# Performance work log

Hardware: AMD Instinct MI355X
Metric: run time of the kernel (lower is better)

Reference implementation:

```python
import jax, jax.numpy as jnp
import numpy as np

N = 50000      # nodes
E = 1_600_000  # edges (avg degree 32)
D = 128        # in/hidden channels
OUT = 64       # out channels


def setup_inputs() -> dict:
    key = jax.random.key(0)
    ks = jax.random.split(key, 12)
    s = 0.08  # ~glorot scale for 128-dim
    return {
        "x": jax.random.normal(ks[0], (N, D), jnp.float32),
        "edge_index": jax.random.randint(ks[1], (2, E), 0, N, dtype=jnp.int64),
        # GCN layer 1
        "W1": jax.random.normal(ks[2], (D, D), jnp.float32) * s,
        "b1": jnp.zeros((D,), jnp.float32),
        # GraphSAGE layer 2 (mean aggregation): lin_l on neighbors, lin_r on root
        "Wl": jax.random.normal(ks[3], (D, D), jnp.float32) * s,
        "Wr": jax.random.normal(ks[4], (D, D), jnp.float32) * s,
        "bs": jnp.zeros((D,), jnp.float32),
        # GAT layer 3 (heads=1, concat=False)
        "Wg": jax.random.normal(ks[5], (D, D), jnp.float32) * s,
        "a_s": jax.random.normal(ks[6], (D,), jnp.float32) * s,
        "a_d": jax.random.normal(ks[7], (D,), jnp.float32) * s,
        "bg": jnp.zeros((D,), jnp.float32),
        # GCN output layer
        "Wo": jax.random.normal(ks[8], (D, OUT), jnp.float32) * s,
        "bo": jnp.zeros((OUT,), jnp.float32),
    }


def _self_loops(src, dst, n):
    loop = jnp.arange(n, dtype=src.dtype)
    return jnp.concatenate([src, loop]), jnp.concatenate([dst, loop])


def gcn_conv(x, W, b, src, dst, n):
    # PyG GCNConv: add self-loops, symmetric normalization D^-1/2 (A+I) D^-1/2
    s2, d2 = _self_loops(src, dst, n)
    deg = jax.ops.segment_sum(jnp.ones_like(d2, dtype=x.dtype), d2, num_segments=n)
    dinv = jnp.where(deg > 0, jax.lax.rsqrt(deg), 0.0)
    h = x @ W                         # [n, out]
    norm = dinv[s2] * dinv[d2]        # [E+n]
    out = jax.ops.segment_sum(h[s2] * norm[:, None], d2, num_segments=n)
    return out + b


def sage_conv(x, Wl, Wr, b, src, dst, n):
    # PyG SAGEConv, aggr='mean': W_l * mean_neigh + W_r * x (no self-loops)
    deg = jax.ops.segment_sum(jnp.ones_like(dst, dtype=x.dtype), dst, num_segments=n)
    agg = jax.ops.segment_sum(x[src], dst, num_segments=n)
    mean = agg / jnp.maximum(deg, 1.0)[:, None]
    return mean @ Wl + x @ Wr + b


def gat_conv(x, W, a_s, a_d, b, src, dst, n):
    # PyG GATConv heads=1, concat=False: self-loops, edge softmax over incoming edges
    h = x @ W                               # [n, out]
    s2, d2 = _self_loops(src, dst, n)
    alpha_src = h @ a_s                     # [n]
    alpha_dst = h @ a_d                     # [n]
    e = jax.nn.leaky_relu(alpha_src[s2] + alpha_dst[d2], negative_slope=0.2)
    m = jax.ops.segment_max(e, d2, num_segments=n)   # every node has a self-loop
    ex = jnp.exp(e - m[d2])
    denom = jax.ops.segment_sum(ex, d2, num_segments=n)
    alpha = ex / denom[d2]
    out = jax.ops.segment_sum(alpha[:, None] * h[s2], d2, num_segments=n)
    return out + b


def reference(x, edge_index, W1, b1, Wl, Wr, bs, Wg, a_s, a_d, bg, Wo, bo):
    src, dst = edge_index[0], edge_index[1]
    n = x.shape[0]
    # eval mode: F.dropout(training=False) is identity
    h = jax.nn.relu(gcn_conv(x, W1, b1, src, dst, n))
    h = jax.nn.relu(sage_conv(h, Wl, Wr, bs, src, dst, n))
    h = jax.nn.relu(gat_conv(h, Wg, a_s, a_d, bg, src, dst, n))
    return gcn_conv(h, Wo, bo, src, dst, n)
```

## Files before the change

kernel.cpp:

```cpp
#include <hip/hip_runtime.h>
#include <math.h>


#define BUCKET_BITS 8
#define BUCKET_SZ   256
#define NBMAX       256
#define CAP         10240
#define CAPE        768

typedef short short8 __attribute__((ext_vector_type(8)));
typedef float f32x4 __attribute__((ext_vector_type(4)));
typedef float f32x2 __attribute__((ext_vector_type(2)));
typedef unsigned int u32x4 __attribute__((ext_vector_type(4)));
typedef unsigned short u16x8 __attribute__((ext_vector_type(8)));

__device__ __forceinline__ float leaky02(float x) { return x > 0.0f ? x : 0.2f * x; }
__device__ __forceinline__ float bflo(unsigned u) { return __uint_as_float(u << 16); }
__device__ __forceinline__ float bfhi(unsigned u) { return __uint_as_float(u & 0xFFFF0000u); }
__device__ __forceinline__ unsigned short f2bf(float f) {
    unsigned u = __float_as_uint(f);
    u += 0x7FFFu + ((u >> 16) & 1u);
    return (unsigned short)(u >> 16);
}

__global__ __launch_bounds__(256) void wpackall_k(
    const float* __restrict__ W1, const float* __restrict__ Wl,
    const float* __restrict__ Wr, const float* __restrict__ Wg,
    const float* __restrict__ Wo,
    unsigned* __restrict__ P1, unsigned* __restrict__ Pl,
    unsigned* __restrict__ Pr, unsigned* __restrict__ Pg,
    unsigned* __restrict__ Po, int* __restrict__ bcur, int nb)
{
    const int b = blockIdx.x;
    if (b == 5) {
        int t = threadIdx.x;
        if (t < nb) bcur[t] = t * CAP;
        return;
    }
    const float* W; unsigned* P; int NO;
    if      (b == 0) { W = W1; P = P1; NO = 128; }
    else if (b == 1) { W = Wl; P = Pl; NO = 128; }
    else if (b == 2) { W = Wr; P = Pr; NO = 128; }
    else if (b == 3) { W = Wg; P = Pg; NO = 128; }
    else             { W = Wo; P = Po; NO = 64;  }
    const int CT = NO / 16;
    const int n4w = NO / 4;
    for (int f = threadIdx.x; f < 64 * n4w; f += 256) {
        const int kp = f / n4w;
        const int n4 = f % n4w;
        const float4 a = *(const float4*)(W + (size_t)(2 * kp) * NO + n4 * 4);
        const float4 bb = *(const float4*)(W + (size_t)(2 * kp + 1) * NO + n4 * 4);
        const int k = 2 * kp, kb = k >> 5, qq = (k >> 3) & 3, p = (k & 7) >> 1;
        const float av[4] = {a.x, a.y, a.z, a.w};
        const float bv[4] = {bb.x, bb.y, bb.z, bb.w};
#pragma unroll
        for (int j = 0; j < 4; j++) {
            int col = n4 * 4 + j;
            int c = col >> 4, nl = col & 15;
            unsigned pk = (unsigned)f2bf(av[j]) | ((unsigned)f2bf(bv[j]) << 16);
            P[(((kb * CT + c) * 64) + qq * 16 + nl) * 4 + p] = pk;
        }
    }
}

template<int NO, bool AFP32, bool SCALE, bool BIASRELU, bool DUAL, bool DOTS>
__global__ __launch_bounds__(256) void mgemm_k(
    const void* __restrict__ Av, const unsigned short* __restrict__ Bp,
    const void* __restrict__ A1v, const unsigned short* __restrict__ Bp1,
    unsigned short* __restrict__ C16,
    const float* __restrict__ scale, const float* __restrict__ bias,
    const float* __restrict__ a_s, const float* __restrict__ a_d,
    float* __restrict__ as_, float* __restrict__ ad_, int n)
{
    constexpr int CT = NO / 16;
    const int tid = threadIdx.x;
    const int wave = tid >> 6, lane = tid & 63;
    const int q = lane >> 4, ml = lane & 15;
    const int row0 = blockIdx.x * 64 + wave * 16;
    int arow = row0 + ml; if (arow >= n) arow = n - 1;

    f32x4 acc[CT];
#pragma unroll
    for (int c = 0; c < CT; c++) acc[c] = {0.f, 0.f, 0.f, 0.f};

    for (int half = 0; half < (DUAL ? 2 : 1); half++) {
        const unsigned short* __restrict__ Bsrc = half ? Bp1 : Bp;
        const void* Asrc = half ? A1v : Av;
#pragma unroll
        for (int kb = 0; kb < 4; kb++) {
            short8 afr;
            if (AFP32) {
                const float* Af = (const float*)Asrc + (size_t)arow * 128 + kb * 32 + q * 8;
                float4 f0 = *(const float4*)Af;
                float4 f1 = *(const float4*)(Af + 4);
                afr[0] = (short)f2bf(f0.x); afr[1] = (short)f2bf(f0.y);
                afr[2] = (short)f2bf(f0.z); afr[3] = (short)f2bf(f0.w);
                afr[4] = (short)f2bf(f1.x); afr[5] = (short)f2bf(f1.y);
                afr[6] = (short)f2bf(f1.z); afr[7] = (short)f2bf(f1.w);
            } else {
                afr = *(const short8*)((const unsigned short*)Asrc +
                                       ((size_t)(kb >> 1) * n + arow) * 64 +
                                       (kb & 1) * 32 + q * 8);
            }
            short8 bfr[CT];
#pragma unroll
            for (int c = 0; c < CT; c++)
                bfr[c] = *(const short8*)(Bsrc + ((size_t)(kb * CT + c) * 64 + lane) * 8);
#pragma unroll
            for (int c = 0; c < CT; c++)
                acc[c] = __builtin_amdgcn_mfma_f32_16x16x32_bf16(afr, bfr[c], acc[c], 0, 0, 0);
        }
    }

    if (DOTS) {
        float ps[4] = {0.f, 0.f, 0.f, 0.f}, pd[4] = {0.f, 0.f, 0.f, 0.f};
#pragma unroll
        for (int c = 0; c < CT; c++) {
            float sv = a_s[c * 16 + ml], dv = a_d[c * 16 + ml];
#pragma unroll
            for (int r = 0; r < 4; r++) {
                ps[r] = fmaf(acc[c][r], sv, ps[r]);
                pd[r] = fmaf(acc[c][r], dv, pd[r]);
            }
        }
#pragma unroll
        for (int off = 1; off < 16; off <<= 1) {
#pragma unroll
            for (int r = 0; r < 4; r++) {
                ps[r] += __shfl_xor(ps[r], off, 64);
                pd[r] += __shfl_xor(pd[r], off, 64);
            }
        }
        if (ml == 0) {
#pragma unroll
            for (int r = 0; r < 4; r++) {
                int row = row0 + q * 4 + r;
                if (row < n) { as_[row] = ps[r]; ad_[row] = pd[r]; }
            }
        }
    }

    float sc[4];
    if (SCALE) {
#pragma unroll
        for (int r = 0; r < 4; r++) {
            int row = row0 + q * 4 + r;
            sc[r] = scale[row < n ? row : 0];
        }
    }
#pragma unroll
    for (int c = 0; c < CT; c++) {
        float bv = BIASRELU ? bias[c * 16 + ml] : 0.0f;
        const int col = c * 16 + ml;
#pragma unroll
        for (int r = 0; r < 4; r++) {
            int row = row0 + q * 4 + r;
            if (row < n) {
                float v = acc[c][r];
                if (SCALE) v *= sc[r];
                if (BIASRELU) v = fmaxf(v + bv, 0.0f);
                C16[((size_t)(col >> 6) * n + row) * 64 + (col & 63)] = f2bf(v);
            }
        }
    }
}

#define PART_CH 4096
__global__ __launch_bounds__(256) void part_k(
    const int* __restrict__ src, const int* __restrict__ dst,
    int* __restrict__ bcur, unsigned long long* __restrict__ part, int nE)
{
    __shared__ int cnt[NBMAX];
    __shared__ int cur[NBMAX];
    const int base = blockIdx.x * PART_CH;
    const int t = threadIdx.x;
    cnt[t] = 0;
    __syncthreads();
    int d[PART_CH / 256], s[PART_CH / 256];
#pragma unroll
    for (int j = 0; j < PART_CH / 256; j++) {
        int e = base + j * 256 + t;
        if (e < nE) {
            d[j] = dst[e]; s[j] = src[e];
            atomicAdd(&cnt[d[j] >> BUCKET_BITS], 1);
        } else d[j] = -1;
    }
    __syncthreads();
    {
        int c = cnt[t];
        cur[t] = c ? atomicAdd(&bcur[t], c) : 0;
    }
    __syncthreads();
#pragma unroll
    for (int j = 0; j < PART_CH / 256; j++) {
        if (d[j] >= 0) {
            int p = atomicAdd(&cur[d[j] >> BUCKET_BITS], 1);
            part[p] = ((unsigned long long)(unsigned)d[j] << 32) | (unsigned)s[j];
        }
    }
}

__global__ __launch_bounds__(256) void csr_k(
    const unsigned long long* __restrict__ part, const int* __restrict__ bcur,
    int* __restrict__ rowptr, int* __restrict__ srcs,
    float* __restrict__ dinv, float* __restrict__ invm, int n, int nE, int nb)
{
    __shared__ int lcnt[BUCKET_SZ];
    __shared__ int sm[BUCKET_SZ];
    __shared__ int lcur[BUCKET_SZ];
    const int b = blockIdx.x;
    const int t = threadIdx.x;
    const int base_in = b * CAP;
    const int cntE = bcur[b] - base_in;

    int vb = (t < nb) ? (bcur[t] - t * CAP) : 0;
    sm[t] = vb;
    __syncthreads();
    for (int off = 1; off < 256; off <<= 1) {
        int tv = (t >= off) ? sm[t - off] : 0;
        __syncthreads();
        sm[t] += tv;
        __syncthreads();
    }
    const int base_out = sm[b] - (bcur[b] - b * CAP);
    __syncthreads();

    lcnt[t] = 0;
    __syncthreads();
#pragma unroll 4
    for (int e = t; e < cntE; e += 256) {
        int dl = (int)(part[base_in + e] >> 32) & (BUCKET_SZ - 1);
        atomicAdd(&lcnt[dl], 1);
    }
    __syncthreads();
    int v = lcnt[t];
    sm[t] = v;
    __syncthreads();
    for (int off = 1; off < 256; off <<= 1) {
        int tv = (t >= off) ? sm[t - off] : 0;
        __syncthreads();
        sm[t] += tv;
        __syncthreads();
    }
    const int excl = sm[t] - v;
    const int node = (b << BUCKET_BITS) + t;
    if (node < n) {
        rowptr[node] = base_out + excl;
        float dg = (float)v;
        dinv[node] = rsqrtf(dg + 1.0f);
        invm[node] = 1.0f / fmaxf(dg, 1.0f);
        if (node == n - 1) rowptr[n] = nE;
    }
    lcur[t] = excl;
    __syncthreads();
#pragma unroll 4
    for (int e = t; e < cntE; e += 256) {
        unsigned long long w = part[base_in + e];
        int dl = (int)(w >> 32) & (BUCKET_SZ - 1);
        int pos = atomicAdd(&lcur[dl], 1);
        srcs[base_out + pos] = (int)(unsigned)w;
    }
}

__global__ __launch_bounds__(256) void gatw_k(
    const int* __restrict__ rowptr, const int* __restrict__ srcs,
    const float* __restrict__ as_, const float* __restrict__ ad_,
    float* __restrict__ ew, float* __restrict__ rdn_, float* __restrict__ sw_, int n)
{
    const int node = blockIdx.x * 32 + (threadIdx.x >> 3);
    const int lane = threadIdx.x & 7;
    if (node >= n) return;
    const int beg = rowptr[node], end = rowptr[node + 1];
    const float ad_d = ad_[node];
    float psum = 0.f;
    for (int k = beg + lane; k < end; k += 8) {
        float e = __expf(leaky02(as_[srcs[k]] + ad_d));
        ew[k] = e;
        psum += e;
    }
#pragma unroll
    for (int off = 4; off > 0; off >>= 1) psum += __shfl_xor(psum, off, 64);
    if (lane == 0) {
        float se = __expf(leaky02(as_[node] + ad_d));
        float r = 1.0f / (psum + se);
        rdn_[node] = r;
        sw_[node] = se * r;
    }
}

template<int MODE, bool OV>
__device__ __forceinline__ void gath_loop(
    const char* __restrict__ Hb, unsigned loff,
    const int* __restrict__ srcs, const float* __restrict__ ew,
    const int* lsrc, const float* lw,
    int beg, int end, int beg_blk, f32x2* acc)
{
    int k = beg;
    for (; k + 16 <= end; k += 16) {
        int s[16]; float wv[16];
#pragma unroll
        for (int j = 0; j < 16; j++) {
            int ofs = k + j - beg_blk;
            if (OV) {
                bool in = ofs < CAPE;
                int ofc = in ? ofs : 0;
                s[j] = in ? lsrc[ofc] : srcs[k + j];
                if (MODE == 2) wv[j] = in ? lw[ofc] : ew[k + j];
            } else {
                s[j] = lsrc[ofs];
                if (MODE == 2) wv[j] = lw[ofs];
            }
        }
        u32x4 h[16];
#pragma unroll
        for (int j = 0; j < 16; j++)
            h[j] = *(const u32x4*)(Hb + (size_t)(((unsigned)s[j] << 7) + loff));
#pragma unroll
        for (int j = 0; j < 16; j++) {
            f32x2 w2 = {wv[j], wv[j]};
#pragma unroll
            for (int c = 0; c < 4; c++) {
                f32x2 hv = {bflo(h[j][c]), bfhi(h[j][c])};
                if (MODE == 2) acc[c] = w2 * hv + acc[c];
                else           acc[c] = acc[c] + hv;
            }
        }
    }
    for (; k + 8 <= end; k += 8) {
        int s[8]; float wv[8];
#pragma unroll
        for (int j = 0; j < 8; j++) {
            int ofs = k + j - beg_blk;
            if (OV) {
                bool in = ofs < CAPE;
                int ofc = in ? ofs : 0;
                s[j] = in ? lsrc[ofc] : srcs[k + j];
                if (MODE == 2) wv[j] = in ? lw[ofc] : ew[k + j];
            } else {
                s[j] = lsrc[ofs];
                if (MODE == 2) wv[j] = lw[ofs];
            }
        }
        u32x4 h[8];
#pragma unroll
        for (int j = 0; j < 8; j++)
            h[j] = *(const u32x4*)(Hb + (size_t)(((unsigned)s[j] << 7) + loff));
#pragma unroll
        for (int j = 0; j < 8; j++) {
            f32x2 w2 = {wv[j], wv[j]};
#pragma unroll
            for (int c = 0; c < 4; c++) {
                f32x2 hv = {bflo(h[j][c]), bfhi(h[j][c])};
                if (MODE == 2) acc[c] = w2 * hv + acc[c];
                else           acc[c] = acc[c] + hv;
            }
        }
    }
    if (k < end) {
        int s[8]; float wv[8];
#pragma unroll
        for (int j = 0; j < 8; j++) {
            int kk = k + j;
            bool act = kk < end;
            int kc = act ? kk : end - 1;
            int ofs = kc - beg_blk;
            int sj; float w0 = 1.0f;
            if (OV) {
                bool in = ofs < CAPE;
                int ofc = in ? ofs : 0;
                sj = in ? lsrc[ofc] : srcs[kc];
                if (MODE == 2) w0 = in ? lw[ofc] : ew[kc];
            } else {
                sj = lsrc[ofs];
                if (MODE == 2) w0 = lw[ofs];
            }
            s[j] = sj;
            wv[j] = act ? ((MODE == 2) ? w0 : 1.0f) : 0.0f;
        }
        u32x4 h[8];
#pragma unroll
        for (int j = 0; j < 8; j++)
            h[j] = *(const u32x4*)(Hb + (size_t)(((unsigned)s[j] << 7) + loff));
#pragma unroll
        for (int j = 0; j < 8; j++) {
            f32x2 w2 = {wv[j], wv[j]};
#pragma unroll
            for (int c = 0; c < 4; c++) {
                f32x2 hv = {bflo(h[j][c]), bfhi(h[j][c])};
                acc[c] = w2 * hv + acc[c];
            }
        }
    }
}

template<int NCB, int MODE>
__global__ __launch_bounds__(128, 4) void gatherbf_k(
    const unsigned short* __restrict__ H16, float* __restrict__ outf,
    unsigned short* __restrict__ out16,
    const int* __restrict__ rowptr, const int* __restrict__ srcs,
    const float* __restrict__ scl,
    const float* __restrict__ sw_,
    const float* __restrict__ ew,
    const float* __restrict__ bias, int n)
{
    constexpr int XPC = 8 / NCB;
    constexpr int NPB = 16;
    __shared__ int lsrc[CAPE];
    __shared__ float lw[(MODE == 2) ? CAPE : 1];

    const int bid = (int)blockIdx.x;
    const int xj = bid & 7;
    const int cb = xj / XPC;
    const int NG = (n + NPB - 1) / NPB;
    const int ng = (bid >> 3) * XPC + (xj % XPC);
    if (ng >= NG) return;

    const int tid = (int)threadIdx.x;
    const int node0 = ng * NPB;
    const int nodeN = min(node0 + NPB, n);
    const int beg_blk = rowptr[node0];
    const int end_blk = rowptr[nodeN];
    const int cnt = end_blk - beg_blk;
    const int cl = min(cnt, CAPE);
    for (int i = tid; i < cl; i += 128) {
        lsrc[i] = srcs[beg_blk + i];
        if (MODE == 2) lw[i] = ew[beg_blk + i];
    }
    __syncthreads();

    const int node = node0 + (tid >> 3);
    const int lane = tid & 7;
    if (node >= nodeN) return;
    const int beg = rowptr[node], end = rowptr[node + 1];
    const char* __restrict__ Hb = (const char*)H16 + (size_t)cb * n * 128;
    const unsigned loff = (unsigned)lane * 16u;

    f32x2 acc[4];
#pragma unroll
    for (int c = 0; c < 4; c++) acc[c] = {0.f, 0.f};

    if (cnt <= CAPE)
        gath_loop<MODE, false>(Hb, loff, srcs, ew, lsrc, lw, beg, end, beg_blk, acc);
    else
        gath_loop<MODE, true>(Hb, loff, srcs, ew, lsrc, lw, beg, end, beg_blk, acc);

    const size_t orow = ((size_t)cb * n + node) * 8 + lane;
    float r[8];
    if (MODE == 0) {
        float sc = scl[node];
#pragma unroll
        for (int c = 0; c < 4; c++) { r[2*c] = acc[c].x * sc; r[2*c+1] = acc[c].y * sc; }
    } else {
        u32x4 su = *(const u32x4*)(Hb + (size_t)(((unsigned)node << 7) + loff));
        float sv[8];
#pragma unroll
        for (int c = 0; c < 4; c++) { sv[2*c] = bflo(su[c]); sv[2*c+1] = bfhi(su[c]); }
        const float4* b4 = (const float4*)bias;
        float4 ba = b4[cb * 16 + lane * 2], bb = b4[cb * 16 + lane * 2 + 1];
        float bv[8] = {ba.x, ba.y, ba.z, ba.w, bb.x, bb.y, bb.z, bb.w};
        float a8[8];
#pragma unroll
        for (int c = 0; c < 4; c++) { a8[2*c] = acc[c].x; a8[2*c+1] = acc[c].y; }
        if (MODE == 2) {
            float rden = scl[node], sw = sw_[node];
#pragma unroll
            for (int j = 0; j < 8; j++)
                r[j] = fmaxf(fmaf(rden, a8[j], fmaf(sw, sv[j], bv[j])), 0.f);
        } else {
            float dv = scl[node];
#pragma unroll
            for (int j = 0; j < 8; j++) {
                r[j] = dv * (a8[j] + sv[j]) + bv[j];
                if (MODE == 1) r[j] = fmaxf(r[j], 0.f);
            }
        }
    }
    if (MODE == 3) {
        float4* o4 = (float4*)(outf + (size_t)node * 64 + lane * 8);
        float4 ra = {r[0], r[1], r[2], r[3]}, rb = {r[4], r[5], r[6], r[7]};
        o4[0] = ra; o4[1] = rb;
    } else {
        u16x8 qv;
#pragma unroll
        for (int j = 0; j < 8; j++) qv[j] = f2bf(r[j]);
        ((u16x8*)out16)[orow] = qv;
    }
}

extern "C" void kernel_launch(void* const* d_in, const int* in_sizes, int n_in,
                              void* d_out, int out_size, void* d_ws, size_t ws_size,
                              hipStream_t stream)
{
    const float* x   = (const float*)d_in[0];
    const int*   ei  = (const int*)d_in[1];
    const float* W1  = (const float*)d_in[2];
    const float* b1  = (const float*)d_in[3];
    const float* Wl  = (const float*)d_in[4];
    const float* Wr  = (const float*)d_in[5];
    const float* bs  = (const float*)d_in[6];
    const float* Wg  = (const float*)d_in[7];
    const float* a_s = (const float*)d_in[8];
    const float* a_d = (const float*)d_in[9];
    const float* bg  = (const float*)d_in[10];
    const float* Wo  = (const float*)d_in[11];
    const float* bo  = (const float*)d_in[12];

    const int n  = in_sizes[0] / 128;
    const int nE = in_sizes[1] / 2;
    const int* src = ei;
    const int* dst = ei + nE;

    char* w = (char*)d_ws;
    auto alloc = [&](size_t bytes) { char* p = w; w += (bytes + 255) & ~(size_t)255; return p; };
    unsigned short* S0 = (unsigned short*)alloc((size_t)n * 128 * 2);
    unsigned short* S1 = (unsigned short*)alloc((size_t)n * 128 * 2);
    unsigned short* S2 = (unsigned short*)alloc((size_t)n * 128 * 2);
    const int nbv = (n + BUCKET_SZ - 1) / BUCKET_SZ;
    unsigned long long* part = (unsigned long long*)alloc((size_t)nbv * CAP * 8);
    int*   srcs   = (int*)alloc((size_t)nE * 4);
    float* ew     = (float*)alloc((size_t)nE * 4);
    int*   rowptr = (int*)alloc((size_t)(n + 1) * 4);
    int*   bcur   = (int*)alloc(NBMAX * 4);
    float* dinv   = (float*)alloc((size_t)n * 4);
    float* invm   = (float*)alloc((size_t)n * 4);
    float* as_    = (float*)alloc((size_t)n * 4);
    float* ad_    = (float*)alloc((size_t)n * 4);
    float* rdn_   = (float*)alloc((size_t)n * 4);
    float* sw_    = (float*)alloc((size_t)n * 4);
    unsigned* P1  = (unsigned*)alloc(64 * 128 * 4);
    unsigned* Pl  = (unsigned*)alloc(64 * 128 * 4);
    unsigned* Pr  = (unsigned*)alloc(64 * 128 * 4);
    unsigned* Pg  = (unsigned*)alloc(64 * 128 * 4);
    unsigned* Po  = (unsigned*)alloc(64 * 64 * 4);

    const int TB = 256;
    auto cdiv = [](long long a, long long b) { return (int)((a + b - 1) / b); };
    const int nb     = nbv;
    const int gPart  = cdiv(nE, PART_CH);
    const int gGemm  = cdiv(n, 64);
    const int NG     = cdiv(n, 16);
    const int gGa128 = 8 * cdiv(NG, 4);
    const int gGa64  = 8 * cdiv(NG, 8);
    const int gGatw  = cdiv(n, 32);

    wpackall_k<<<6, TB, 0, stream>>>(W1, Wl, Wr, Wg, Wo, P1, Pl, Pr, Pg, Po, bcur, nb);
    part_k<<<gPart, TB, 0, stream>>>(src, dst, bcur, part, nE);
    csr_k<<<nb, TB, 0, stream>>>(part, bcur, rowptr, srcs, dinv, invm, n, nE, nb);

    mgemm_k<128, true, true, false, false, false><<<gGemm, TB, 0, stream>>>(
        x, (const unsigned short*)P1, nullptr, nullptr, S0, dinv, nullptr,
        nullptr, nullptr, nullptr, nullptr, n);
    gatherbf_k<2, 1><<<gGa128, 128, 0, stream>>>(S0, nullptr, S1, rowptr, srcs,
                                                 dinv, nullptr, nullptr, b1, n);

    gatherbf_k<2, 0><<<gGa128, 128, 0, stream>>>(S1, nullptr, S0, rowptr, srcs,
                                                 invm, nullptr, nullptr, nullptr, n);
    mgemm_k<128, false, false, true, true, false><<<gGemm, TB, 0, stream>>>(
        S0, (const unsigned short*)Pl, S1, (const unsigned short*)Pr, S2,
        nullptr, bs, nullptr, nullptr, nullptr, nullptr, n);

    mgemm_k<128, false, false, false, false, true><<<gGemm, TB, 0, stream>>>(
        S2, (const unsigned short*)Pg, nullptr, nullptr, S1, nullptr, nullptr,
        a_s, a_d, as_, ad_, n);
    gatw_k<<<gGatw, TB, 0, stream>>>(rowptr, srcs, as_, ad_, ew, rdn_, sw_, n);
    gatherbf_k<2, 2><<<gGa128, 128, 0, stream>>>(S1, nullptr, S0, rowptr, srcs,
                                                 rdn_, sw_, ew, bg, n);

    mgemm_k<64, false, true, false, false, false><<<gGemm, TB, 0, stream>>>(
        S0, (const unsigned short*)Po, nullptr, nullptr, S2, dinv, nullptr,
        nullptr, nullptr, nullptr, nullptr, n);
    gatherbf_k<1, 3><<<gGa64, 128, 0, stream>>>(S2, (float*)d_out, nullptr, rowptr, srcs,
                                                dinv, nullptr, nullptr, bo, n);
}
```

Before: 328.1 us.

## Switch bf16 feature buffers to row-major and gather full rows per node

Replaces the column-blocked bf16 feature layout (two 64-wide column blocks stored as separate planes) with plain row-major storage in the GEMM loads and stores. The gather kernel now gives each node 16 lanes covering its whole 256-byte row (8 lanes for the 64-wide output) in 256-thread blocks, instead of one block per column half. The goal is to read each edge's source index list once per node rather than once per column block, and to fetch whole contiguous rows. The trade-off is fewer blocks with more threads and register pressure each, plus a different shared-memory staging capacity.

Result: slower. 366.5 us (+11.7%).

```diff
diff --git a/kernel.cpp b/kernel.cpp
--- a/kernel.cpp
+++ b/kernel.cpp
@@ -6,7 +6,6 @@
 #define BUCKET_SZ   256
 #define NBMAX       256
 #define CAP         10240
-#define CAPE        768
 
 typedef short short8 __attribute__((ext_vector_type(8)));
 typedef float f32x4 __attribute__((ext_vector_type(4)));
@@ -99,8 +98,7 @@
                 afr[6] = (short)f2bf(f1.z); afr[7] = (short)f2bf(f1.w);
             } else {
                 afr = *(const short8*)((const unsigned short*)Asrc +
-                                       ((size_t)(kb >> 1) * n + arow) * 64 +
-                                       (kb & 1) * 32 + q * 8);
+                                       (size_t)arow * 128 + kb * 32 + q * 8);
             }
             short8 bfr[CT];
 #pragma unroll
@@ -159,7 +157,7 @@
                 float v = acc[c][r];
                 if (SCALE) v *= sc[r];
                 if (BIASRELU) v = fmaxf(v + bv, 0.0f);
-                C16[((size_t)(col >> 6) * n + row) * 64 + (col & 63)] = f2bf(v);
+                C16[(size_t)row * NO + col] = f2bf(v);
             }
         }
     }
@@ -288,13 +286,14 @@
     }
 }
 
-template<int MODE, bool OV>
+template<int LPN, int MODE, int CAPEV, bool OV>
 __device__ __forceinline__ void gath_loop(
     const char* __restrict__ Hb, unsigned loff,
     const int* __restrict__ srcs, const float* __restrict__ ew,
     const int* lsrc, const float* lw,
     int beg, int end, int beg_blk, f32x2* acc)
 {
+    constexpr int RSH = (LPN == 16) ? 8 : 7;
     int k = beg;
     for (; k + 16 <= end; k += 16) {
         int s[16]; float wv[16];
@@ -302,7 +301,7 @@
         for (int j = 0; j < 16; j++) {
             int ofs = k + j - beg_blk;
             if (OV) {
-                bool in = ofs < CAPE;
+                bool in = ofs < CAPEV;
                 int ofc = in ? ofs : 0;
                 s[j] = in ? lsrc[ofc] : srcs[k + j];
                 if (MODE == 2) wv[j] = in ? lw[ofc] : ew[k + j];
@@ -314,7 +313,7 @@
         u32x4 h[16];
 #pragma unroll
         for (int j = 0; j < 16; j++)
-            h[j] = *(const u32x4*)(Hb + (size_t)(((unsigned)s[j] << 7) + loff));
+            h[j] = *(const u32x4*)(Hb + (size_t)(((unsigned)s[j] << RSH) + loff));
 #pragma unroll
         for (int j = 0; j < 16; j++) {
             f32x2 w2 = {wv[j], wv[j]};
@@ -332,7 +331,7 @@
         for (int j = 0; j < 8; j++) {
             int ofs = k + j - beg_blk;
             if (OV) {
-                bool in = ofs < CAPE;
+                bool in = ofs < CAPEV;
                 int ofc = in ? ofs : 0;
                 s[j] = in ? lsrc[ofc] : srcs[k + j];
                 if (MODE == 2) wv[j] = in ? lw[ofc] : ew[k + j];
@@ -344,7 +343,7 @@
         u32x4 h[8];
 #pragma unroll
         for (int j = 0; j < 8; j++)
-            h[j] = *(const u32x4*)(Hb + (size_t)(((unsigned)s[j] << 7) + loff));
+            h[j] = *(const u32x4*)(Hb + (size_t)(((unsigned)s[j] << RSH) + loff));
 #pragma unroll
         for (int j = 0; j < 8; j++) {
             f32x2 w2 = {wv[j], wv[j]};
@@ -366,7 +365,7 @@
             int ofs = kc - beg_blk;
             int sj; float w0 = 1.0f;
             if (OV) {
-                bool in = ofs < CAPE;
+                bool in = ofs < CAPEV;
                 int ofc = in ? ofs : 0;
                 sj = in ? lsrc[ofc] : srcs[kc];
                 if (MODE == 2) w0 = in ? lw[ofc] : ew[kc];
@@ -380,7 +379,7 @@
         u32x4 h[8];
 #pragma unroll
         for (int j = 0; j < 8; j++)
-            h[j] = *(const u32x4*)(Hb + (size_t)(((unsigned)s[j] << 7) + loff));
+            h[j] = *(const u32x4*)(Hb + (size_t)(((unsigned)s[j] << RSH) + loff));
 #pragma unroll
         for (int j = 0; j < 8; j++) {
             f32x2 w2 = {wv[j], wv[j]};
@@ -393,8 +392,8 @@
     }
 }
 
-template<int NCB, int MODE>
-__global__ __launch_bounds__(128, 4) void gatherbf_k(
+template<int LPN, int MODE>
+__global__ __launch_bounds__(256, 4) void gatherbf_k(
     const unsigned short* __restrict__ H16, float* __restrict__ outf,
     unsigned short* __restrict__ out16,
     const int* __restrict__ rowptr, const int* __restrict__ srcs,
@@ -403,60 +402,54 @@
     const float* __restrict__ ew,
     const float* __restrict__ bias, int n)
 {
-    constexpr int XPC = 8 / NCB;
-    constexpr int NPB = 16;
-    __shared__ int lsrc[CAPE];
-    __shared__ float lw[(MODE == 2) ? CAPE : 1];
-
-    const int bid = (int)blockIdx.x;
-    const int xj = bid & 7;
-    const int cb = xj / XPC;
-    const int NG = (n + NPB - 1) / NPB;
-    const int ng = (bid >> 3) * XPC + (xj % XPC);
-    if (ng >= NG) return;
+    constexpr int NPB = 256 / LPN;
+    constexpr int CAPEV = (LPN == 16) ? 768 : 1280;
+    constexpr int RSH = (LPN == 16) ? 8 : 7;
+    __shared__ int lsrc[CAPEV];
+    __shared__ float lw[(MODE == 2) ? CAPEV : 1];
 
     const int tid = (int)threadIdx.x;
-    const int node0 = ng * NPB;
+    const int node0 = (int)blockIdx.x * NPB;
     const int nodeN = min(node0 + NPB, n);
     const int beg_blk = rowptr[node0];
     const int end_blk = rowptr[nodeN];
     const int cnt = end_blk - beg_blk;
-    const int cl = min(cnt, CAPE);
-    for (int i = tid; i < cl; i += 128) {
+    const int cl = min(cnt, CAPEV);
+    for (int i = tid; i < cl; i += 256) {
         lsrc[i] = srcs[beg_blk + i];
         if (MODE == 2) lw[i] = ew[beg_blk + i];
     }
     __syncthreads();
 
-    const int node = node0 + (tid >> 3);
-    const int lane = tid & 7;
+    const int node = node0 + tid / LPN;
+    const int lane = tid & (LPN - 1);
     if (node >= nodeN) return;
     const int beg = rowptr[node], end = rowptr[node + 1];
-    const char* __restrict__ Hb = (const char*)H16 + (size_t)cb * n * 128;
+    const char* __restrict__ Hb = (const char*)H16;
     const unsigned loff = (unsigned)lane * 16u;
 
     f32x2 acc[4];
 #pragma unroll
     for (int c = 0; c < 4; c++) acc[c] = {0.f, 0.f};
 
-    if (cnt <= CAPE)
-        gath_loop<MODE, false>(Hb, loff, srcs, ew, lsrc, lw, beg, end, beg_blk, acc);
+    if (cnt <= CAPEV)
+        gath_loop<LPN, MODE, CAPEV, false>(Hb, loff, srcs, ew, lsrc, lw, beg, end, beg_blk, acc);
     else
-        gath_loop<MODE, true>(Hb, loff, srcs, ew, lsrc, lw, beg, end, beg_blk, acc);
-
-    const size_t orow = ((size_t)cb * n + node) * 8 + lane;
+        gath_loop<LPN, MODE, CAPEV, true>(Hb, loff, srcs, ew, lsrc, lw, beg, end, beg_blk, acc);
+
+    const size_t orow = (size_t)node * LPN + lane;
     float r[8];
     if (MODE == 0) {
         float sc = scl[node];
 #pragma unroll
         for (int c = 0; c < 4; c++) { r[2*c] = acc[c].x * sc; r[2*c+1] = acc[c].y * sc; }
     } else {
-        u32x4 su = *(const u32x4*)(Hb + (size_t)(((unsigned)node << 7) + loff));
+        u32x4 su = *(const u32x4*)(Hb + (size_t)(((unsigned)node << RSH) + loff));
         float sv[8];
 #pragma unroll
         for (int c = 0; c < 4; c++) { sv[2*c] = bflo(su[c]); sv[2*c+1] = bfhi(su[c]); }
         const float4* b4 = (const float4*)bias;
-        float4 ba = b4[cb * 16 + lane * 2], bb = b4[cb * 16 + lane * 2 + 1];
+        float4 ba = b4[lane * 2], bb = b4[lane * 2 + 1];
         float bv[8] = {ba.x, ba.y, ba.z, ba.w, bb.x, bb.y, bb.z, bb.w};
         float a8[8];
 #pragma unroll
@@ -538,9 +531,8 @@
     const int nb     = nbv;
     const int gPart  = cdiv(nE, PART_CH);
     const int gGemm  = cdiv(n, 64);
-    const int NG     = cdiv(n, 16);
-    const int gGa128 = 8 * cdiv(NG, 4);
-    const int gGa64  = 8 * cdiv(NG, 8);
+    const int gGa128 = cdiv(n, 16);
+    const int gGa64  = cdiv(n, 32);
     const int gGatw  = cdiv(n, 32);
 
     wpackall_k<<<6, TB, 0, stream>>>(W1, Wl, Wr, Wg, Wo, P1, Pl, Pr, Pg, Po, bcur, nb);
@@ -550,10 +542,10 @@
     mgemm_k<128, true, true, false, false, false><<<gGemm, TB, 0, stream>>>(
         x, (const unsigned short*)P1, nullptr, nullptr, S0, dinv, nullptr,
         nullptr, nullptr, nullptr, nullptr, n);
-    gatherbf_k<2, 1><<<gGa128, 128, 0, stream>>>(S0, nullptr, S1, rowptr, srcs,
+    gatherbf_k<16, 1><<<gGa128, TB, 0, stream>>>(S0, nullptr, S1, rowptr, srcs,
                                                  dinv, nullptr, nullptr, b1, n);
 
-    gatherbf_k<2, 0><<<gGa128, 128, 0, stream>>>(S1, nullptr, S0, rowptr, srcs,
+    gatherbf_k<16, 0><<<gGa128, TB, 0, stream>>>(S1, nullptr, S0, rowptr, srcs,
                                                  invm, nullptr, nullptr, nullptr, n);
     mgemm_k<128, false, false, true, true, false><<<gGemm, TB, 0, stream>>>(
         S0, (const unsigned short*)Pl, S1, (const unsigned short*)Pr, S2,
@@ -563,12 +555,12 @@
         S2, (const unsigned short*)Pg, nullptr, nullptr, S1, nullptr, nullptr,
         a_s, a_d, as_, ad_, n);
     gatw_k<<<gGatw, TB, 0, stream>>>(rowptr, srcs, as_, ad_, ew, rdn_, sw_, n);
-    gatherbf_k<2, 2><<<gGa128, 128, 0, stream>>>(S1, nullptr, S0, rowptr, srcs,
+    gatherbf_k<16, 2><<<gGa128, TB, 0, stream>>>(S1, nullptr, S0, rowptr, srcs,
                                                  rdn_, sw_, ew, bg, n);
 
     mgemm_k<64, false, true, false, false, false><<<gGemm, TB, 0, stream>>>(
         S0, (const unsigned short*)Po, nullptr, nullptr, S2, dinv, nullptr,
         nullptr, nullptr, nullptr, nullptr, n);
-    gatherbf_k<1, 3><<<gGa64, 128, 0, stream>>>(S2, (float*)d_out, nullptr, rowptr, srcs,
-                                                dinv, nullptr, nullptr, bo, n);
-}
+    gatherbf_k<8, 3><<<gGa64, TB, 0, stream>>>(S2, (float*)d_out, nullptr, rowptr, srcs,
+                                               dinv, nullptr, nullptr, bo, n);
+}
```

## Fuse GAT edge-softmax weight computation into the attention gather kernel

Applied to the files above, without the earlier changes.

Removes the separate gatw_k kernel that wrote per-edge exp weights and per-node softmax denominators to global memory. The MODE 2 gather now computes edge weights into shared memory during staging, using a small binary search over local row offsets, and derives the softmax denominator per node with a warp reduction. This avoids a launch and an edge-sized global write and read. In exchange, the exps and as_ gathers are recomputed in each column-block replica of the gather.

Result: no change. 329.4 us (+0.4%).

```diff
diff --git a/kernel.cpp b/kernel.cpp
--- a/kernel.cpp
+++ b/kernel.cpp
@@ -262,36 +262,10 @@
     }
 }
 
-__global__ __launch_bounds__(256) void gatw_k(
-    const int* __restrict__ rowptr, const int* __restrict__ srcs,
-    const float* __restrict__ as_, const float* __restrict__ ad_,
-    float* __restrict__ ew, float* __restrict__ rdn_, float* __restrict__ sw_, int n)
-{
-    const int node = blockIdx.x * 32 + (threadIdx.x >> 3);
-    const int lane = threadIdx.x & 7;
-    if (node >= n) return;
-    const int beg = rowptr[node], end = rowptr[node + 1];
-    const float ad_d = ad_[node];
-    float psum = 0.f;
-    for (int k = beg + lane; k < end; k += 8) {
-        float e = __expf(leaky02(as_[srcs[k]] + ad_d));
-        ew[k] = e;
-        psum += e;
-    }
-#pragma unroll
-    for (int off = 4; off > 0; off >>= 1) psum += __shfl_xor(psum, off, 64);
-    if (lane == 0) {
-        float se = __expf(leaky02(as_[node] + ad_d));
-        float r = 1.0f / (psum + se);
-        rdn_[node] = r;
-        sw_[node] = se * r;
-    }
-}
-
 template<int MODE, bool OV>
 __device__ __forceinline__ void gath_loop(
     const char* __restrict__ Hb, unsigned loff,
-    const int* __restrict__ srcs, const float* __restrict__ ew,
+    const int* __restrict__ srcs, const float* __restrict__ as_, float ad_d,
     const int* lsrc, const float* lw,
     int beg, int end, int beg_blk, f32x2* acc)
 {
@@ -304,8 +278,10 @@
             if (OV) {
                 bool in = ofs < CAPE;
                 int ofc = in ? ofs : 0;
-                s[j] = in ? lsrc[ofc] : srcs[k + j];
-                if (MODE == 2) wv[j] = in ? lw[ofc] : ew[k + j];
+                int sg = in ? lsrc[ofc] : srcs[k + j];
+                s[j] = sg;
+                if (MODE == 2)
+                    wv[j] = in ? lw[ofc] : __expf(leaky02(as_[sg] + ad_d));
             } else {
                 s[j] = lsrc[ofs];
                 if (MODE == 2) wv[j] = lw[ofs];
@@ -334,8 +310,10 @@
             if (OV) {
                 bool in = ofs < CAPE;
                 int ofc = in ? ofs : 0;
-                s[j] = in ? lsrc[ofc] : srcs[k + j];
-                if (MODE == 2) wv[j] = in ? lw[ofc] : ew[k + j];
+                int sg = in ? lsrc[ofc] : srcs[k + j];
+                s[j] = sg;
+                if (MODE == 2)
+                    wv[j] = in ? lw[ofc] : __expf(leaky02(as_[sg] + ad_d));
             } else {
                 s[j] = lsrc[ofs];
                 if (MODE == 2) wv[j] = lw[ofs];
@@ -369,7 +347,8 @@
                 bool in = ofs < CAPE;
                 int ofc = in ? ofs : 0;
                 sj = in ? lsrc[ofc] : srcs[kc];
-                if (MODE == 2) w0 = in ? lw[ofc] : ew[kc];
+                if (MODE == 2)
+                    w0 = in ? lw[ofc] : __expf(leaky02(as_[sj] + ad_d));
             } else {
                 sj = lsrc[ofs];
                 if (MODE == 2) w0 = lw[ofs];
@@ -398,15 +377,16 @@
     const unsigned short* __restrict__ H16, float* __restrict__ outf,
     unsigned short* __restrict__ out16,
     const int* __restrict__ rowptr, const int* __restrict__ srcs,
-    const float* __restrict__ scl,
-    const float* __restrict__ sw_,
-    const float* __restrict__ ew,
+    const float* __restrict__ p0, const float* __restrict__ p1,
     const float* __restrict__ bias, int n)
 {
     constexpr int XPC = 8 / NCB;
     constexpr int NPB = 16;
     __shared__ int lsrc[CAPE];
     __shared__ float lw[(MODE == 2) ? CAPE : 1];
+    __shared__ int lro[(MODE == 2) ? (NPB + 1) : 1];
+    __shared__ float lad[(MODE == 2) ? NPB : 1];
+    __shared__ float las[(MODE == 2) ? NPB : 1];
 
     const int bid = (int)blockIdx.x;
     const int xj = bid & 7;
@@ -422,11 +402,27 @@
     const int end_blk = rowptr[nodeN];
     const int cnt = end_blk - beg_blk;
     const int cl = min(cnt, CAPE);
-    for (int i = tid; i < cl; i += 128) {
-        lsrc[i] = srcs[beg_blk + i];
-        if (MODE == 2) lw[i] = ew[beg_blk + i];
-    }
-    __syncthreads();
+
+    if (MODE == 2) {
+        if (tid <= nodeN - node0) lro[tid] = rowptr[node0 + tid] - beg_blk;
+        if (tid < nodeN - node0) { lad[tid] = p1[node0 + tid]; las[tid] = p0[node0 + tid]; }
+        __syncthreads();
+        for (int i = tid; i < cl; i += 128) {
+            int s = srcs[beg_blk + i];
+            lsrc[i] = s;
+            int lo = 0, hi = nodeN - node0;
+#pragma unroll
+            for (int st = 0; st < 4; st++) {
+                int mid = (lo + hi) >> 1;
+                if (i >= lro[mid]) lo = mid; else hi = mid;
+            }
+            lw[i] = __expf(leaky02(p0[s] + lad[lo]));
+        }
+        __syncthreads();
+    } else {
+        for (int i = tid; i < cl; i += 128) lsrc[i] = srcs[beg_blk + i];
+        __syncthreads();
+    }
 
     const int node = node0 + (tid >> 3);
     const int lane = tid & 7;
@@ -435,19 +431,36 @@
     const char* __restrict__ Hb = (const char*)H16 + (size_t)cb * n * 128;
     const unsigned loff = (unsigned)lane * 16u;
 
+    float ad_d = 0.f, rden = 0.f, sw = 0.f;
+    if (MODE == 2) {
+        const int nl = node - node0;
+        ad_d = lad[nl];
+        float self_e = __expf(leaky02(las[nl] + ad_d));
+        float psum = 0.f;
+        for (int k = beg + lane; k < end; k += 8) {
+            int ofs = k - beg_blk;
+            psum += (ofs < CAPE) ? lw[ofs]
+                                 : __expf(leaky02(p0[srcs[k]] + ad_d));
+        }
+#pragma unroll
+        for (int off = 4; off > 0; off >>= 1) psum += __shfl_xor(psum, off, 64);
+        rden = 1.0f / (psum + self_e);
+        sw = self_e * rden;
+    }
+
     f32x2 acc[4];
 #pragma unroll
     for (int c = 0; c < 4; c++) acc[c] = {0.f, 0.f};
 
     if (cnt <= CAPE)
-        gath_loop<MODE, false>(Hb, loff, srcs, ew, lsrc, lw, beg, end, beg_blk, acc);
+        gath_loop<MODE, false>(Hb, loff, srcs, p0, ad_d, lsrc, lw, beg, end, beg_blk, acc);
     else
-        gath_loop<MODE, true>(Hb, loff, srcs, ew, lsrc, lw, beg, end, beg_blk, acc);
+        gath_loop<MODE, true>(Hb, loff, srcs, p0, ad_d, lsrc, lw, beg, end, beg_blk, acc);
 
     const size_t orow = ((size_t)cb * n + node) * 8 + lane;
     float r[8];
     if (MODE == 0) {
-        float sc = scl[node];
+        float sc = p0[node];
 #pragma unroll
         for (int c = 0; c < 4; c++) { r[2*c] = acc[c].x * sc; r[2*c+1] = acc[c].y * sc; }
     } else {
@@ -462,12 +475,11 @@
 #pragma unroll
         for (int c = 0; c < 4; c++) { a8[2*c] = acc[c].x; a8[2*c+1] = acc[c].y; }
         if (MODE == 2) {
-            float rden = scl[node], sw = sw_[node];
 #pragma unroll
             for (int j = 0; j < 8; j++)
                 r[j] = fmaxf(fmaf(rden, a8[j], fmaf(sw, sv[j], bv[j])), 0.f);
         } else {
-            float dv = scl[node];
+            float dv = p0[node];
 #pragma unroll
             for (int j = 0; j < 8; j++) {
                 r[j] = dv * (a8[j] + sv[j]) + bv[j];
@@ -518,15 +530,12 @@
     const int nbv = (n + BUCKET_SZ - 1) / BUCKET_SZ;
     unsigned long long* part = (unsigned long long*)alloc((size_t)nbv * CAP * 8);
     int*   srcs   = (int*)alloc((size_t)nE * 4);
-    float* ew     = (float*)alloc((size_t)nE * 4);
     int*   rowptr = (int*)alloc((size_t)(n + 1) * 4);
     int*   bcur   = (int*)alloc(NBMAX * 4);
     float* dinv   = (float*)alloc((size_t)n * 4);
     float* invm   = (float*)alloc((size_t)n * 4);
     float* as_    = (float*)alloc((size_t)n * 4);
     float* ad_    = (float*)alloc((size_t)n * 4);
-    float* rdn_   = (float*)alloc((size_t)n * 4);
-    float* sw_    = (float*)alloc((size_t)n * 4);
     unsigned* P1  = (unsigned*)alloc(64 * 128 * 4);
     unsigned* Pl  = (unsigned*)alloc(64 * 128 * 4);
     unsigned* Pr  = (unsigned*)alloc(64 * 128 * 4);
@@ -541,7 +550,6 @@
     const int NG     = cdiv(n, 16);
     const int gGa128 = 8 * cdiv(NG, 4);
     const int gGa64  = 8 * cdiv(NG, 8);
-    const int gGatw  = cdiv(n, 32);
 
     wpackall_k<<<6, TB, 0, stream>>>(W1, Wl, Wr, Wg, Wo, P1, Pl, Pr, Pg, Po, bcur, nb);
     part_k<<<gPart, TB, 0, stream>>>(src, dst, bcur, part, nE);
@@ -551,10 +559,10 @@
         x, (const unsigned short*)P1, nullptr, nullptr, S0, dinv, nullptr,
         nullptr, nullptr, nullptr, nullptr, n);
     gatherbf_k<2, 1><<<gGa128, 128, 0, stream>>>(S0, nullptr, S1, rowptr, srcs,
-                                                 dinv, nullptr, nullptr, b1, n);
+                                                 dinv, nullptr, b1, n);
 
     gatherbf_k<2, 0><<<gGa128, 128, 0, stream>>>(S1, nullptr, S0, rowptr, srcs,
-                                                 invm, nullptr, nullptr, nullptr, n);
+                                                 invm, nullptr, nullptr, n);
     mgemm_k<128, false, false, true, true, false><<<gGemm, TB, 0, stream>>>(
         S0, (const unsigned short*)Pl, S1, (const unsigned short*)Pr, S2,
         nullptr, bs, nullptr, nullptr, nullptr, nullptr, n);
@@ -562,13 +570,12 @@
     mgemm_k<128, false, false, false, false, true><<<gGemm, TB, 0, stream>>>(
         S2, (const unsigned short*)Pg, nullptr, nullptr, S1, nullptr, nullptr,
         a_s, a_d, as_, ad_, n);
-    gatw_k<<<gGatw, TB, 0, stream>>>(rowptr, srcs, as_, ad_, ew, rdn_, sw_, n);
     gatherbf_k<2, 2><<<gGa128, 128, 0, stream>>>(S1, nullptr, S0, rowptr, srcs,
-                                                 rdn_, sw_, ew, bg, n);
+                                                 as_, ad_, bg, n);
 
     mgemm_k<64, false, true, false, false, false><<<gGemm, TB, 0, stream>>>(
         S0, (const unsigned short*)Po, nullptr, nullptr, S2, dinv, nullptr,
         nullptr, nullptr, nullptr, nullptr, n);
     gatherbf_k<1, 3><<<gGa64, 128, 0, stream>>>(S2, (float*)d_out, nullptr, rowptr, srcs,
-                                                dinv, nullptr, nullptr, bo, n);
-}
+                                                dinv, nullptr, bo, n);
+}
```
